# Performance work log

Measured on AMD Instinct MI355X. Metric: run time of the kernel, lower is better.

## Reference

```python
import jax, jax.numpy as jnp
import numpy as np

HEADS = 8

def _conv1x1(x, W, b):
    # x: [n, Cin, H, W]; W: [Cout, Cin]; b: [Cout]
    return jnp.einsum('nchw,oc->nohw', x, W) + b[None, :, None, None]

def setup_inputs() -> dict:
    key = jax.random.key(0)
    ks = jax.random.split(key, 11)
    n, Cin, H, W = 8, 256, 80, 80
    Ck, Cv = 256, 256
    s_in = 1.0 / np.sqrt(Cin)
    s_v = 1.0 / np.sqrt(Cv)
    return {
        'query_feature': jax.random.normal(ks[0], (n, Cin, H, W), jnp.float32),
        'key_feature': jax.random.normal(ks[1], (n, Cin, H, W), jnp.float32),
        'value_feature': jax.random.normal(ks[2], (n, Cin, H, W), jnp.float32),
        'Wq': jax.random.normal(ks[3], (Ck, Cin), jnp.float32) * s_in,
        'bq': jax.random.normal(ks[4], (Ck,), jnp.float32) * s_in,
        'Wk': jax.random.normal(ks[5], (Ck, Cin), jnp.float32) * s_in,
        'bk': jax.random.normal(ks[6], (Ck,), jnp.float32) * s_in,
        'Wv': jax.random.normal(ks[7], (Cv, Cin), jnp.float32) * s_in,
        'bv': jax.random.normal(ks[8], (Cv,), jnp.float32) * s_in,
        'Wr': jax.random.normal(ks[9], (Cin, Cv), jnp.float32) * s_v,
        'br': jax.random.normal(ks[10], (Cin,), jnp.float32) * s_v,
    }

def reference(query_feature, key_feature, value_feature, Wq, bq, Wk, bk, Wv, bv, Wr, br):
    n, _, qh, qw = query_feature.shape
    kvn, _, kvh, kvw = key_feature.shape
    Ck = Wq.shape[0]
    Cv = Wv.shape[0]
    hk = Ck // HEADS
    hv = Cv // HEADS
    Lq = qh * qw
    Lkv = kvh * kvw
    # 1x1 conv projections, split channels into heads (consecutive channel blocks)
    q = _conv1x1(query_feature, Wq, bq).reshape(n, HEADS, hk, Lq)
    k = _conv1x1(key_feature, Wk, bk).reshape(kvn, HEADS, hk, Lkv)
    v = _conv1x1(value_feature, Wv, bv).reshape(kvn, HEADS, hv, Lkv)
    # softmax: keys over spatial positions, queries over head channels
    k = jax.nn.softmax(k, axis=3)
    q = jax.nn.softmax(q, axis=2)
    # efficient (linear) attention: context = K @ V^T, out = context^T @ Q
    context = jnp.einsum('nhkl,nhvl->nhkv', k, v)          # [n, H, hk, hv]
    attended = jnp.einsum('nhkv,nhkl->nhvl', context, q)   # [n, H, hv, Lq]
    aggregated = attended.reshape(n, Cv, qh, qw)
    return _conv1x1(aggregated, Wr, br) + query_feature
```

## Files before the change

### kernel.cpp

```cpp
#include <hip/hip_runtime.h>
#include <hip/hip_bf16.h>

#define NB 8
#define C 256
#define LL 6400
#define HEADS 8
#define HC 32
#define NH 64
#define SEG 40
#define SL 160
#define QPP 264

typedef unsigned short u16;
typedef unsigned int u32;
typedef __attribute__((ext_vector_type(8))) short bf16x8;
typedef __attribute__((ext_vector_type(4))) float f32x4;

typedef __attribute__((address_space(1))) const u32 ga_u32;
typedef __attribute__((address_space(3))) u32 ls_u32;

__device__ __forceinline__ void gload_lds16(const u16* g, u16* l) {
  __builtin_amdgcn_global_load_lds((ga_u32*)g, (ls_u32*)l, 16, 0, 0);
}

__device__ __forceinline__ float bf2f(u32 u) { return __uint_as_float(u << 16); }
__device__ __forceinline__ u16 f2bf(float f) {
  __hip_bfloat16 h = __float2bfloat16(f);
  return *(u16*)&h;
}
__device__ __forceinline__ void unpack8(uint4 u, float* f) {
  f[0] = bf2f(u.x & 0xffffu); f[1] = bf2f(u.x >> 16);
  f[2] = bf2f(u.y & 0xffffu); f[3] = bf2f(u.y >> 16);
  f[4] = bf2f(u.z & 0xffffu); f[5] = bf2f(u.z >> 16);
  f[6] = bf2f(u.w & 0xffffu); f[7] = bf2f(u.w >> 16);
}

struct WcvtArgs { const float* W[3]; u16* Wb[3]; };
struct PFArgs { const float* X[3]; const u16* Wb[3]; const float* bias[3]; u16* P[3]; };

__global__ __launch_bounds__(256) void wcvt(WcvtArgs a) {
  const int idx = blockIdx.x * 256 + threadIdx.x;
  const int which = idx >> 13, r = idx & 8191;
  const int co = r >> 5, c8 = r & 31;
  const float* src = a.W[which] + co * 256 + c8 * 8;
  float4 v0 = *(const float4*)src, v1 = *(const float4*)(src + 4);
  union { bf16x8 v; u16 h[8]; } o;
  o.h[0] = f2bf(v0.x); o.h[1] = f2bf(v0.y); o.h[2] = f2bf(v0.z); o.h[3] = f2bf(v0.w);
  o.h[4] = f2bf(v1.x); o.h[5] = f2bf(v1.y); o.h[6] = f2bf(v1.z); o.h[7] = f2bf(v1.w);
  const int p = (c8 & ~3) | ((c8 & 3) ^ ((co >> 1) & 3));
  *(bf16x8*)&a.Wb[which][co * 256 + p * 8] = o.v;
}

__global__ __launch_bounds__(256, 2) void proj_fused(PFArgs args) {
  __shared__ __align__(16) float Xs[64 * 64];
  __shared__ __align__(16) u16 Ap[64 * 256];
  __shared__ __align__(16) u16 Bs[2][256 * 32];
  const int which = blockIdx.y >> 3, n = blockIdx.y & 7;
  const int l0 = blockIdx.x * 64;
  const int t = threadIdx.x;
  const int lane = t & 63, wave = t >> 6;
  const int fr = lane & 15, q = lane >> 4;
  const int wl = (wave & 1) * 32, wco = (wave >> 1) * 128;
  const int srow = t >> 2, scol = (t & 3) * 8;
  const float* X = args.X[which] + (size_t)n * C * LL;
  const u16* Wb = args.Wb[which];

#pragma unroll
  for (int s = 0; s < 4; ++s)
    gload_lds16(&Wb[(size_t)(s * 64 + srow) * C + scol], &Bs[0][s * 2048 + wave * 512]);

#pragma unroll
  for (int qt = 0; qt < 4; ++qt) {
#pragma unroll
    for (int s = 0; s < 4; ++s) {
      const int r = wave * 16 + s * 4;
      gload_lds16((const u16*)&X[(size_t)(qt * 64 + r + (lane >> 4)) * LL + l0 + (lane & 15) * 4],
                  (u16*)&Xs[r * 64]);
    }
    __syncthreads();
#pragma unroll
    for (int g = 0; g < 2; ++g) {
      const int cg = wave * 2 + g;
      float v[8];
#pragma unroll
      for (int e = 0; e < 8; ++e) v[e] = Xs[(cg * 8 + e) * 64 + lane];
      union { uint4 u; u32 w[4]; } pk;
#pragma unroll
      for (int p = 0; p < 4; ++p)
        pk.w[p] = (u32)f2bf(v[2 * p]) | ((u32)f2bf(v[2 * p + 1]) << 16);
      const int cb = qt * 8 + cg;
      *(uint4*)&Ap[lane * 256 + (cb ^ (lane & 7)) * 8] = pk.u;
    }
    __syncthreads();
  }

  f32x4 acc[2][8] = {};
  const int sco = (fr >> 1) & 3;
#pragma unroll
  for (int kt = 0; kt < 8; ++kt) {
    if (kt < 7) {
#pragma unroll
      for (int s = 0; s < 4; ++s)
        gload_lds16(&Wb[(size_t)(s * 64 + srow) * C + (kt + 1) * 32 + scol],
                    &Bs[(kt + 1) & 1][s * 2048 + wave * 512]);
    }
    bf16x8 a[2];
#pragma unroll
    for (int i = 0; i < 2; ++i) {
      const int row = wl + i * 16 + fr;
      a[i] = *(const bf16x8*)&Ap[row * 256 + (((kt * 4 + q) ^ (row & 7)) * 8)];
    }
#pragma unroll
    for (int j = 0; j < 8; ++j) {
      bf16x8 b = *(const bf16x8*)&Bs[kt & 1][(wco + j * 16 + fr) * 32 + ((q ^ sco) * 8)];
#pragma unroll
      for (int i = 0; i < 2; ++i)
        acc[i][j] = __builtin_amdgcn_mfma_f32_16x16x32_bf16(a[i], b, acc[i][j], 0, 0, 0);
    }
    __syncthreads();
  }

  const float* bias = args.bias[which];
  u16* P = args.P[which] + (size_t)n * LL * C;
  float bb[8];
#pragma unroll
  for (int j = 0; j < 8; ++j) bb[j] = bias[wco + j * 16 + fr];
#pragma unroll
  for (int i = 0; i < 2; ++i)
#pragma unroll
    for (int r = 0; r < 4; ++r) {
      const int lrow = wl + i * 16 + q * 4 + r;
#pragma unroll
      for (int j = 0; j < 8; ++j)
        Ap[lrow * 256 + wco + j * 16 + fr] = f2bf(acc[i][j][r] + bb[j]);
    }
  __syncthreads();
  const int rg = t >> 5, ch = t & 31;
#pragma unroll
  for (int s = 0; s < 8; ++s) {
    const int row = rg * 8 + s;
    bf16x8 vrow = *(const bf16x8*)&Ap[row * 256 + ch * 8];
    *(bf16x8*)&P[(size_t)(l0 + row) * C + ch * 8] = vrow;
  }
}

__global__ __launch_bounds__(256) void ctx_part(const u16* __restrict__ Kt,
    const u16* __restrict__ Vt, float* __restrict__ pctx, float* __restrict__ psum) {
  __shared__ __align__(16) u16 Ks[16 * 256];
  __shared__ __align__(16) u16 Vs[16 * 256];
  const int seg = blockIdx.x, n = blockIdx.y;
  const int t = threadIdx.x, lane = t & 63, wave = t >> 6;
  const int l0 = seg * SL;
  const u16* KtN = Kt + (size_t)n * LL * C;
  const u16* VtN = Vt + (size_t)n * LL * C;
  const int k4 = (lane & 7) * 4, v8 = lane >> 3;
  float acc[2][4][4] = {};
  float ssum[2][4] = {};
  for (int ls = 0; ls < SL; ls += 16) {
    __syncthreads();
#pragma unroll
    for (int i = 0; i < 2; ++i) {
      const int r = wave * 4 + i * 2;
      gload_lds16(&KtN[(size_t)(l0 + ls + r) * C + lane * 8], &Ks[r * 256]);
      gload_lds16(&VtN[(size_t)(l0 + ls + r) * C + lane * 8], &Vs[r * 256]);
    }
    __syncthreads();
#pragma unroll
    for (int hh = 0; hh < 2; ++hh) {
      const int h = wave * 2 + hh;
#pragma unroll
      for (int l = 0; l < 16; ++l) {
        ushort4 ku = *(const ushort4*)&Ks[l * 256 + h * 32 + k4];
        ushort4 vu = *(const ushort4*)&Vs[l * 256 + h * 32 + v8 * 4];
        float ek[4] = {__expf(bf2f(ku.x)), __expf(bf2f(ku.y)),
                       __expf(bf2f(ku.z)), __expf(bf2f(ku.w))};
        float vf[4] = {bf2f(vu.x), bf2f(vu.y), bf2f(vu.z), bf2f(vu.w)};
#pragma unroll
        for (int i = 0; i < 4; ++i)
#pragma unroll
          for (int j = 0; j < 4; ++j) acc[hh][i][j] = fmaf(ek[i], vf[j], acc[hh][i][j]);
        if (v8 == 0)
#pragma unroll
          for (int i = 0; i < 4; ++i) ssum[hh][i] += ek[i];
      }
    }
  }
#pragma unroll
  for (int hh = 0; hh < 2; ++hh) {
    const int h = wave * 2 + hh;
    const size_t pb = ((size_t)seg * NH + n * 8 + h) * 1024;
#pragma unroll
    for (int i = 0; i < 4; ++i)
#pragma unroll
      for (int j = 0; j < 4; ++j)
        pctx[pb + (size_t)(k4 + i) * 32 + v8 * 4 + j] = acc[hh][i][j];
    if (v8 == 0) {
      const size_t sb = ((size_t)seg * NH + n * 8 + h) * 32;
#pragma unroll
      for (int i = 0; i < 4; ++i) psum[sb + k4 + i] = ssum[hh][i];
    }
  }
}

__global__ __launch_bounds__(256) void ctx_reduce(const float* __restrict__ pctx,
    const float* __restrict__ psum, float* __restrict__ ctx) {
  const int idx = blockIdx.x * 256 + threadIdx.x;
  const int nh = idx >> 10, e = idx & 1023, k = e >> 5;
  float s = 0.f, ss = 0.f;
  for (int g = 0; g < SEG; ++g) {
    s += pctx[(size_t)(g * NH + nh) * 1024 + e];
    ss += psum[(size_t)(g * NH + nh) * 32 + k];
  }
  ctx[idx] = s / ss;
}

__global__ __launch_bounds__(256) void mfuse(const float* __restrict__ Wr,
    const float* __restrict__ ctx, u16* __restrict__ M) {
  const int idx = blockIdx.x * 256 + threadIdx.x;
  const int hk = idx & 255;
  const int o = (idx >> 8) & 255;
  const int n = idx >> 16;
  const int h = hk >> 5, k = hk & 31;
  const float* wr = Wr + (size_t)o * C + h * HC;
  const float* cx = ctx + ((size_t)(n * HEADS + h) * HC + k) * HC;
  float s = 0.f;
#pragma unroll
  for (int v = 0; v < HC; ++v) s = fmaf(wr[v], cx[v], s);
  M[idx] = f2bf(s);
}

__global__ __launch_bounds__(256) void out_fused(const u16* __restrict__ Qt,
    const u16* __restrict__ Mb, const float* __restrict__ br,
    const float* __restrict__ Xq, float* __restrict__ out) {
  __shared__ __align__(16) u16 Qp[64 * QPP];
  __shared__ __align__(16) u16 As[2][128 * 32];
  const int n = blockIdx.y, l0 = blockIdx.x * 64;
  const int t = threadIdx.x, lane = t & 63, wave = t >> 6;
  const int fr = lane & 15, q = lane >> 4;
  const int wcoL = (wave >> 1) * 64, wl = (wave & 1) * 32;
  const int srow = t >> 2, scol = (t & 3) * 8;
  const u16* QtN = Qt + (size_t)n * LL * C;
  const u16* MbN = Mb + (size_t)n * C * C;

#pragma unroll
  for (int s = 0; s < 2; ++s)
    gload_lds16(&MbN[(size_t)(s * 64 + srow) * C + scol], &As[0][s * 2048 + wave * 512]);

#pragma unroll
  for (int p = 0; p < 2; ++p) {
    const int row = p * 32 + (t >> 3);
    const int g = t & 7;
    const uint4* src = (const uint4*)&QtN[(size_t)(l0 + row) * C + g * 32];
    uint4 u0 = src[0], u1 = src[1], u2 = src[2], u3 = src[3];
    float v[32];
    unpack8(u0, v); unpack8(u1, v + 8); unpack8(u2, v + 16); unpack8(u3, v + 24);
    float e[32], s = 0.f;
#pragma unroll
    for (int j = 0; j < 32; ++j) { e[j] = __expf(v[j]); s += e[j]; }
    const float r = 1.0f / s;
    uint4* drow = (uint4*)&Qp[row * QPP + g * 32];
#pragma unroll
    for (int b4 = 0; b4 < 4; ++b4) {
      union { uint4 u; u16 h[8]; } o;
#pragma unroll
      for (int j = 0; j < 8; ++j) o.h[j] = f2bf(e[b4 * 8 + j] * r);
      drow[b4] = o.u;
    }
  }
  asm volatile("s_waitcnt vmcnt(0) lgkmcnt(0)" ::: "memory");
  __builtin_amdgcn_s_barrier();
  __builtin_amdgcn_sched_barrier(0);

  f32x4 acc[2][4][2] = {};
#pragma unroll
  for (int it = 0; it < 16; ++it) {
    const int coh = it >> 3, k0 = (it & 7) * 32, cur = it & 1;
    if (it < 15) {
      const int nco = (it + 1) >> 3, nk0 = ((it + 1) & 7) * 32;
#pragma unroll
      for (int s = 0; s < 2; ++s)
        gload_lds16(&MbN[(size_t)(nco * 128 + s * 64 + srow) * C + nk0 + scol],
                    &As[cur ^ 1][s * 2048 + wave * 512]);
      __builtin_amdgcn_sched_barrier(0);
    }
    bf16x8 a[4], b[2];
#pragma unroll
    for (int i = 0; i < 4; ++i)
      a[i] = *(const bf16x8*)&As[cur][(wcoL + i * 16 + fr) * 32 + q * 8];
#pragma unroll
    for (int j = 0; j < 2; ++j)
      b[j] = *(const bf16x8*)&Qp[(wl + j * 16 + fr) * QPP + k0 + q * 8];
#pragma unroll
    for (int i = 0; i < 4; ++i)
#pragma unroll
      for (int j = 0; j < 2; ++j)
        acc[coh][i][j] = __builtin_amdgcn_mfma_f32_16x16x32_bf16(a[i], b[j], acc[coh][i][j], 0, 0, 0);
    if (it < 15) {
      asm volatile("s_waitcnt vmcnt(0) lgkmcnt(0)" ::: "memory");
      __builtin_amdgcn_s_barrier();
      __builtin_amdgcn_sched_barrier(0);
    }
  }

  const float* XqN = Xq + (size_t)n * C * LL;
  float* On = out + (size_t)n * C * LL;
#pragma unroll
  for (int coh = 0; coh < 2; ++coh)
#pragma unroll
    for (int i = 0; i < 4; ++i)
#pragma unroll
      for (int r = 0; r < 4; ++r) {
        const int co = coh * 128 + wcoL + i * 16 + q * 4 + r;
        const float bb = br[co];
#pragma unroll
        for (int j = 0; j < 2; ++j) {
          const int l = l0 + wl + j * 16 + fr;
          const size_t off = (size_t)co * LL + l;
          On[off] = acc[coh][i][j][r] + bb + XqN[off];
        }
      }
}

extern "C" void kernel_launch(void* const* d_in, const int* in_sizes, int n_in,
                              void* d_out, int out_size, void* d_ws, size_t ws_size,
                              hipStream_t stream) {
  const float* Xq = (const float*)d_in[0];
  const float* Xk = (const float*)d_in[1];
  const float* Xv = (const float*)d_in[2];
  const float* Wq = (const float*)d_in[3];
  const float* bq = (const float*)d_in[4];
  const float* Wk = (const float*)d_in[5];
  const float* bk = (const float*)d_in[6];
  const float* Wv = (const float*)d_in[7];
  const float* bv = (const float*)d_in[8];
  const float* Wr = (const float*)d_in[9];
  const float* br = (const float*)d_in[10];
  float* out = (float*)d_out;

  char* ws = (char*)d_ws;
  const size_t nelem = (size_t)NB * LL * C;
  u16* Qt = (u16*)ws;
  u16* Kt = (u16*)(ws + nelem * 2);
  u16* Vt = (u16*)(ws + nelem * 4);
  char* p = ws + nelem * 6;
  u16* Wqb = (u16*)p; p += C * C * 2;
  u16* Wkb = (u16*)p; p += C * C * 2;
  u16* Wvb = (u16*)p; p += C * C * 2;
  float* pctx = (float*)p; p += (size_t)SEG * NH * HC * HC * 4;
  float* psum = (float*)p; p += (size_t)SEG * NH * HC * 4;
  float* ctx = (float*)p;  p += (size_t)NH * HC * HC * 4;
  u16* Mb = (u16*)p;

  WcvtArgs wa;
  wa.W[0] = Wq; wa.W[1] = Wk; wa.W[2] = Wv;
  wa.Wb[0] = Wqb; wa.Wb[1] = Wkb; wa.Wb[2] = Wvb;
  wcvt<<<96, 256, 0, stream>>>(wa);

  PFArgs pa;
  pa.X[0] = Xq; pa.X[1] = Xk; pa.X[2] = Xv;
  pa.Wb[0] = Wqb; pa.Wb[1] = Wkb; pa.Wb[2] = Wvb;
  pa.bias[0] = bq; pa.bias[1] = bk; pa.bias[2] = bv;
  pa.P[0] = Qt; pa.P[1] = Kt; pa.P[2] = Vt;
  proj_fused<<<dim3(100, 24), 256, 0, stream>>>(pa);

  ctx_part<<<dim3(SEG, NB), 256, 0, stream>>>(Kt, Vt, pctx, psum);
  ctx_reduce<<<NH * HC * HC / 256, 256, 0, stream>>>(pctx, psum, ctx);
  mfuse<<<NB * C * C / 256, 256, 0, stream>>>(Wr, ctx, Mb);
  out_fused<<<dim3(100, NB), 256, 0, stream>>>(Qt, Mb, br, Xq, out);
}
```

Measured before the change: 334.6 us.

## Double-buffer global-to-LDS loads in projection and context kernels

The projection kernel's X staging changes from four 64-channel tiles, each with full block barriers, to eight 32-channel double-buffered stages. Each wave waits on its own vmcnt and prefetches two stages ahead. The ctx_part K/V tiles are likewise double-buffered, issuing the next tile's async LDS loads before computing on the current one. This aims to hide global memory latency behind conversion and FMA work, at the cost of more LDS and reliance on hand-placed waitcnt and barrier ordering.

```diff
diff --git a/kernel.cpp b/kernel.cpp
--- a/kernel.cpp
+++ b/kernel.cpp
@@ -52,7 +52,7 @@
 }
 
 __global__ __launch_bounds__(256, 2) void proj_fused(PFArgs args) {
-  __shared__ __align__(16) float Xs[64 * 64];
+  __shared__ __align__(16) float Xs[2][32 * 64];
   __shared__ __align__(16) u16 Ap[64 * 256];
   __shared__ __align__(16) u16 Bs[2][256 * 32];
   const int which = blockIdx.y >> 3, n = blockIdx.y & 7;
@@ -64,35 +64,43 @@
   const int srow = t >> 2, scol = (t & 3) * 8;
   const float* X = args.X[which] + (size_t)n * C * LL;
   const u16* Wb = args.Wb[which];
+  const int xr = lane >> 4, xc = (lane & 15) * 4;
 
 #pragma unroll
   for (int s = 0; s < 4; ++s)
     gload_lds16(&Wb[(size_t)(s * 64 + srow) * C + scol], &Bs[0][s * 2048 + wave * 512]);
 
-#pragma unroll
-  for (int qt = 0; qt < 4; ++qt) {
-#pragma unroll
-    for (int s = 0; s < 4; ++s) {
-      const int r = wave * 16 + s * 4;
-      gload_lds16((const u16*)&X[(size_t)(qt * 64 + r + (lane >> 4)) * LL + l0 + (lane & 15) * 4],
-                  (u16*)&Xs[r * 64]);
-    }
-    __syncthreads();
-#pragma unroll
-    for (int g = 0; g < 2; ++g) {
-      const int cg = wave * 2 + g;
-      float v[8];
-#pragma unroll
-      for (int e = 0; e < 8; ++e) v[e] = Xs[(cg * 8 + e) * 64 + lane];
-      union { uint4 u; u32 w[4]; } pk;
-#pragma unroll
-      for (int p = 0; p < 4; ++p)
-        pk.w[p] = (u32)f2bf(v[2 * p]) | ((u32)f2bf(v[2 * p + 1]) << 16);
-      const int cb = qt * 8 + cg;
-      *(uint4*)&Ap[lane * 256 + (cb ^ (lane & 7)) * 8] = pk.u;
-    }
-    __syncthreads();
-  }
+#define PF_STAGE(e)                                                                  \
+  {                                                                                  \
+    _Pragma("unroll")                                                                \
+    for (int s = 0; s < 2; ++s)                                                      \
+      gload_lds16((const u16*)&X[(size_t)(32 * (e) + wave * 8 + s * 4 + xr) * LL +   \
+                                 l0 + xc],                                           \
+                  (u16*)&Xs[(e) & 1][(wave * 8 + s * 4) * 64]);                      \
+  }
+  PF_STAGE(0)
+  PF_STAGE(1)
+#pragma unroll
+  for (int e = 0; e < 8; ++e) {
+    if (e < 7) { asm volatile("s_waitcnt vmcnt(2)" ::: "memory"); }
+    else       { asm volatile("s_waitcnt vmcnt(0)" ::: "memory"); }
+    float v[8];
+#pragma unroll
+    for (int ei = 0; ei < 8; ++ei) v[ei] = Xs[e & 1][(wave * 8 + ei) * 64 + lane];
+    union { uint4 u; u32 w[4]; } pk;
+#pragma unroll
+    for (int p = 0; p < 4; ++p)
+      pk.w[p] = (u32)f2bf(v[2 * p]) | ((u32)f2bf(v[2 * p + 1]) << 16);
+    const int cb = e * 4 + wave;
+    *(uint4*)&Ap[lane * 256 + ((cb ^ (lane & 7)) * 8)] = pk.u;
+    if (e < 6) {
+      asm volatile("s_waitcnt lgkmcnt(0)" ::: "memory");
+      __builtin_amdgcn_sched_barrier(0);
+      PF_STAGE(e + 2)
+    }
+  }
+#undef PF_STAGE
+  __syncthreads();
 
   f32x4 acc[2][8] = {};
   const int sco = (fr >> 1) & 3;
@@ -146,8 +154,8 @@
 
 __global__ __launch_bounds__(256) void ctx_part(const u16* __restrict__ Kt,
     const u16* __restrict__ Vt, float* __restrict__ pctx, float* __restrict__ psum) {
-  __shared__ __align__(16) u16 Ks[16 * 256];
-  __shared__ __align__(16) u16 Vs[16 * 256];
+  __shared__ __align__(16) u16 Ks[2][16 * 256];
+  __shared__ __align__(16) u16 Vs[2][16 * 256];
   const int seg = blockIdx.x, n = blockIdx.y;
   const int t = threadIdx.x, lane = t & 63, wave = t >> 6;
   const int l0 = seg * SL;
@@ -156,22 +164,34 @@
   const int k4 = (lane & 7) * 4, v8 = lane >> 3;
   float acc[2][4][4] = {};
   float ssum[2][4] = {};
-  for (int ls = 0; ls < SL; ls += 16) {
-    __syncthreads();
-#pragma unroll
-    for (int i = 0; i < 2; ++i) {
-      const int r = wave * 4 + i * 2;
-      gload_lds16(&KtN[(size_t)(l0 + ls + r) * C + lane * 8], &Ks[r * 256]);
-      gload_lds16(&VtN[(size_t)(l0 + ls + r) * C + lane * 8], &Vs[r * 256]);
-    }
-    __syncthreads();
+
+#define CP_STAGE(it)                                                              \
+  {                                                                               \
+    _Pragma("unroll")                                                             \
+    for (int i = 0; i < 2; ++i) {                                                 \
+      const int r = wave * 4 + i * 2;                                             \
+      gload_lds16(&KtN[(size_t)(l0 + (it) * 16 + r) * C + lane * 8],              \
+                  &Ks[(it) & 1][r * 256]);                                        \
+      gload_lds16(&VtN[(size_t)(l0 + (it) * 16 + r) * C + lane * 8],              \
+                  &Vs[(it) & 1][r * 256]);                                        \
+    }                                                                             \
+  }
+  CP_STAGE(0)
+#pragma unroll
+  for (int it = 0; it < 10; ++it) {
+    if (it < 9) CP_STAGE(it + 1)
+    if (it < 9) { asm volatile("s_waitcnt vmcnt(4)" ::: "memory"); }
+    else        { asm volatile("s_waitcnt vmcnt(0)" ::: "memory"); }
+    __builtin_amdgcn_s_barrier();
+    const u16* Kc = Ks[it & 1];
+    const u16* Vc = Vs[it & 1];
 #pragma unroll
     for (int hh = 0; hh < 2; ++hh) {
       const int h = wave * 2 + hh;
 #pragma unroll
       for (int l = 0; l < 16; ++l) {
-        ushort4 ku = *(const ushort4*)&Ks[l * 256 + h * 32 + k4];
-        ushort4 vu = *(const ushort4*)&Vs[l * 256 + h * 32 + v8 * 4];
+        ushort4 ku = *(const ushort4*)&Kc[l * 256 + h * 32 + k4];
+        ushort4 vu = *(const ushort4*)&Vc[l * 256 + h * 32 + v8 * 4];
         float ek[4] = {__expf(bf2f(ku.x)), __expf(bf2f(ku.y)),
                        __expf(bf2f(ku.z)), __expf(bf2f(ku.w))};
         float vf[4] = {bf2f(vu.x), bf2f(vu.y), bf2f(vu.z), bf2f(vu.w)};
@@ -184,7 +204,10 @@
           for (int i = 0; i < 4; ++i) ssum[hh][i] += ek[i];
       }
     }
-  }
+    __builtin_amdgcn_s_barrier();
+  }
+#undef CP_STAGE
+
 #pragma unroll
   for (int hh = 0; hh < 2; ++hh) {
     const int h = wave * 2 + hh;
```

Result: slower. 1.099 ms (+228.5%).
